# Kernel optimization log

Hardware: AMD Instinct MI355X
Metric: run time of the kernel (lower is better)

Reference implementation:

```python
import jax, jax.numpy as jnp
import numpy as np

B, N, D = 4, 2048, 1024
H, A, Lv = 8, 128, 128   # heads, attention_dim (qk), linear_dim (v)
NUM_BLOCKS = 4
QKV_W = (2 * Lv + 2 * A) * H  # 4096
NEG = -1e9


def setup_inputs() -> dict:
    key = jax.random.key(0)
    ks = jax.random.split(key, 10)
    past_lengths = jax.random.randint(ks[0], (B,), 0, N)
    past_ids = jax.random.randint(ks[1], (B, N), 0, 10000)
    past_embeddings = jax.random.normal(ks[2], (B, N, D), dtype=jnp.float32)
    # per-block parameters, stacked on leading block axis (xavier-ish scale)
    qkv_w = jax.random.normal(ks[3], (NUM_BLOCKS, D, QKV_W), dtype=jnp.float32) * (1.0 / np.sqrt(D))
    qkv_b = jnp.zeros((NUM_BLOCKS, QKV_W), dtype=jnp.float32)
    out_w = jax.random.normal(ks[4], (NUM_BLOCKS, Lv * H, D), dtype=jnp.float32) * (1.0 / np.sqrt(Lv * H))
    out_b = jnp.zeros((NUM_BLOCKS, D), dtype=jnp.float32)
    ln_g = jnp.ones((NUM_BLOCKS, D), dtype=jnp.float32)
    ln_b = jnp.zeros((NUM_BLOCKS, D), dtype=jnp.float32)
    return {"past_lengths": past_lengths, "past_ids": past_ids,
            "past_embeddings": past_embeddings, "qkv_w": qkv_w, "qkv_b": qkv_b,
            "out_w": out_w, "out_b": out_b, "ln_g": ln_g, "ln_b": ln_b}


def _layer_norm(x, g, b, eps=1e-5):
    mu = jnp.mean(x, axis=-1, keepdims=True)
    var = jnp.mean(jnp.square(x - mu), axis=-1, keepdims=True)
    return (x - mu) * jax.lax.rsqrt(var + eps) * g + b


def _block(x, mask, qw, qb, ow, ob, g, b):
    xn = _layer_norm(x, g, b)
    qkv = (xn @ qw + qb).reshape(B, N, H, 2 * Lv + 2 * A)
    q = qkv[..., :A]              # [B,N,H,A]
    k = qkv[..., A:2 * A]         # [B,N,H,A]
    v = qkv[..., 2 * A:2 * A + Lv]  # [B,N,H,Lv]
    scores = jnp.einsum('bnha,bmha->bhnm', q, k) / np.sqrt(A)
    # original: masked_fill(-inf) -> silu -> /N -> softmax; we mask after the
    # silu transform with a large-negative logit so masked weights are ~0
    logits = jnp.where(mask[:, None, :, :], jax.nn.silu(scores) / N, NEG)
    w = jax.nn.softmax(logits, axis=-1)
    attn = jnp.einsum('bhnm,bmhl->bnhl', w, v).reshape(B, N, H * Lv)
    return x + attn @ ow + ob


def reference(past_lengths, past_ids, past_embeddings, qkv_w, qkv_b, out_w, out_b, ln_g, ln_b):
    valid = past_ids != 0                                   # [B,N]
    causal = jnp.triu(jnp.ones((N, N), dtype=bool), k=1)     # faithful to buffer (triu, diag=1)
    mask = causal[None] & valid[:, None, :] & valid[:, :, None]  # [B,N,N]
    x = past_embeddings
    for i in range(NUM_BLOCKS):
        x = _block(x, mask, qkv_w[i], qkv_b[i], out_w[i], out_b[i], ln_g[i], ln_b[i])
    return x
```

## Files before the change

### kernel.cpp

```cpp
#include <hip/hip_runtime.h>

typedef __bf16 bf16_t;
typedef __bf16 bf16x8 __attribute__((ext_vector_type(8)));
typedef __bf16 bf16x4 __attribute__((ext_vector_type(4)));
typedef float f32x4 __attribute__((ext_vector_type(4)));
typedef unsigned int u32x4 __attribute__((ext_vector_type(4)));

#define B_ 4
#define N_ 2048
#define D_ 1024
#define H_ 8
#define NB_ 4
#define M_ (B_*N_)
#define QN_ 3072
#define QKN_ 2048

__device__ __forceinline__ void async_copy16(const void* gsrc, void* ldst) {
    __builtin_amdgcn_global_load_lds(
        (const __attribute__((address_space(1))) void*)gsrc,
        (__attribute__((address_space(3))) void*)ldst, 16, 0, 0);
}

static constexpr size_t WT_OFF  = 0;
static constexpr size_t WT_SZ   = (size_t)NB_*QN_*D_*2;
static constexpr size_t OWT_OFF = WT_OFF + WT_SZ;
static constexpr size_t OWT_SZ  = (size_t)NB_*D_*D_*2;
static constexpr size_t XN_OFF  = OWT_OFF + OWT_SZ;
static constexpr size_t XN_SZ   = (size_t)M_*D_*2;
static constexpr size_t QK_OFF  = XN_OFF + XN_SZ;
static constexpr size_t QK_SZ   = (size_t)M_*QKN_*2;
static constexpr size_t VT_OFF  = QK_OFF + QK_SZ;
static constexpr size_t VT_SZ   = (size_t)32*128*N_*2;
static constexpr size_t ATT_OFF = VT_OFF + VT_SZ;
static constexpr size_t ATT_SZ  = (size_t)M_*D_*2;
static constexpr size_t QBR_OFF = ATT_OFF + ATT_SZ;
static constexpr size_t QBR_SZ  = (size_t)NB_*QN_*4;
static constexpr size_t VS_OFF  = QBR_OFF + QBR_SZ;
static constexpr size_t VS_SZ   = (size_t)NB_*32*128*4;
static constexpr size_t MASK_OFF = VS_OFF + VS_SZ;

__global__ __launch_bounds__(256) void repack_qkvw(const float* __restrict__ qw, bf16_t* __restrict__ wt)
{
    __shared__ float tile[64][65];
    const int nb = blockIdx.z;
    const int j0 = blockIdx.x * 64, d0 = blockIdx.y * 64;
    const int tx = threadIdx.x, ty = threadIdx.y;
    const float* src = qw + (size_t)nb * D_ * 4096;
    const int jj = j0 + tx;
    const int sel = jj >> 10, rr = jj & 1023, hh = rr >> 7, aa = rr & 127;
    const int orig = hh * 512 + sel * 128 + aa;
#pragma unroll
    for (int it = 0; it < 16; ++it) {
        int dr = it * 4 + ty;
        tile[dr][tx] = src[(size_t)(d0 + dr) * 4096 + orig];
    }
    __syncthreads();
    bf16_t* dst = wt + (size_t)nb * QN_ * D_;
#pragma unroll
    for (int it = 0; it < 16; ++it) {
        int jr = it * 4 + ty;
        dst[(size_t)(j0 + jr) * D_ + d0 + tx] = (bf16_t)tile[tx][jr];
    }
}

__global__ __launch_bounds__(256) void repack_outw(const float* __restrict__ ow, bf16_t* __restrict__ owt)
{
    __shared__ float tile[64][65];
    const int nb = blockIdx.z;
    const int j0 = blockIdx.x * 64, d0 = blockIdx.y * 64;
    const int tx = threadIdx.x, ty = threadIdx.y;
    const float* src = ow + (size_t)nb * D_ * D_;
#pragma unroll
    for (int it = 0; it < 16; ++it) {
        int dr = it * 4 + ty;
        tile[dr][tx] = src[(size_t)(d0 + dr) * D_ + j0 + tx];
    }
    __syncthreads();
    bf16_t* dst = owt + (size_t)nb * D_ * D_;
#pragma unroll
    for (int it = 0; it < 16; ++it) {
        int jr = it * 4 + ty;
        dst[(size_t)(j0 + jr) * D_ + d0 + tx] = (bf16_t)tile[tx][jr];
    }
}

__global__ __launch_bounds__(256) void repack_qb(const float* __restrict__ qb, float* __restrict__ qbr)
{
    int idx = blockIdx.x * 256 + threadIdx.x;
    int nb = idx / QN_, jj = idx % QN_;
    int sel = jj >> 10, rr = jj & 1023, hh = rr >> 7, aa = rr & 127;
    qbr[idx] = qb[nb * 4096 + hh * 512 + sel * 128 + aa];
}

__global__ __launch_bounds__(256) void mask_kernel(const int* __restrict__ past_ids, unsigned short* __restrict__ maskA,
                                                   float* __restrict__ vsl)
{
    const int idx = blockIdx.x * 256 + threadIdx.x;
    vsl[idx] = 0.f; vsl[idx + 8192] = 0.f;
    const int b = idx >> 11, P = idx & 2047;
    const int k = P & 31;
    const int m = (P & ~31) | (((k >> 2) & 1) << 4) | (((k >> 3) & 3) << 2) | (k & 3);
    maskA[idx] = past_ids[b * N_ + m] != 0 ? 0xFFFFu : 0u;
}

__global__ __launch_bounds__(256) void ln_kernel(const float* __restrict__ x, const float* __restrict__ g,
                                                 const float* __restrict__ bb, bf16_t* __restrict__ xn)
{
    const int row = blockIdx.x, tid = threadIdx.x;
    const float4 v = ((const float4*)(x + (size_t)row * D_))[tid];
    float s = v.x + v.y + v.z + v.w;
    float q = v.x * v.x + v.y * v.y + v.z * v.z + v.w * v.w;
#pragma unroll
    for (int d = 32; d >= 1; d >>= 1) { s += __shfl_xor(s, d); q += __shfl_xor(q, d); }
    __shared__ float ls[4], lq[4];
    if ((tid & 63) == 0) { ls[tid >> 6] = s; lq[tid >> 6] = q; }
    __syncthreads();
    s = ls[0] + ls[1] + ls[2] + ls[3];
    q = lq[0] + lq[1] + lq[2] + lq[3];
    const float mean = s * (1.f / 1024.f);
    const float var  = q * (1.f / 1024.f) - mean * mean;
    const float inv  = rsqrtf(var + 1e-5f);
    const float4 gg = ((const float4*)g)[tid];
    const float4 bv = ((const float4*)bb)[tid];
    bf16x4 o;
    o[0] = (bf16_t)((v.x - mean) * inv * gg.x + bv.x);
    o[1] = (bf16_t)((v.y - mean) * inv * gg.y + bv.y);
    o[2] = (bf16_t)((v.z - mean) * inv * gg.z + bv.z);
    o[3] = (bf16_t)((v.w - mean) * inv * gg.w + bv.w);
    *(bf16x4*)(xn + (size_t)row * D_ + tid * 4) = o;
}

__global__ __launch_bounds__(512, 2) void gemm_qkv(const bf16_t* __restrict__ Am, const bf16_t* __restrict__ Bt,
                                                   const float* __restrict__ bias,
                                                   bf16_t* __restrict__ outQK, bf16_t* __restrict__ vtOut,
                                                   float* __restrict__ vsOut)
{
    __shared__ bf16_t As[4 * 8192];
    __shared__ bf16_t Bs[4 * 6144];
    const int tid = threadIdx.x;
    const int lane = tid & 63, wave = tid >> 6;
    const int wr = wave >> 2, wc = wave & 3;
    const int quad = lane >> 4, l15 = lane & 15;
    const int swz = quad ^ ((l15 >> 1) & 3);
    const int slane8 = ((lane & 3) ^ ((lane >> 3) & 3)) * 8;
    const int lrow = lane >> 2;
    const int m0 = blockIdx.y * 256, n0 = blockIdx.x * 192;
    const int Kn = D_;
    const bool w4 = (wave < 4);

    const int ch = wave * 2;
    const int bch0 = w4 ? 2 * wave : 4 + wave;
    const int bch1 = w4 ? 2 * wave + 1 : bch0;
    const bf16_t* gA0 = Am + (size_t)(m0 + ch * 16 + lrow) * Kn + slane8;
    const bf16_t* gA1 = gA0 + (size_t)16 * Kn;
    const bf16_t* gB0 = Bt + (size_t)(n0 + bch0 * 16 + lrow) * Kn + slane8;
    const bf16_t* gB1 = Bt + (size_t)(n0 + bch1 * 16 + lrow) * Kn + slane8;
    bf16_t* const dA0 = &As[ch * 512 + lane * 8];
    bf16_t* const dA1 = &As[(ch + 1) * 512 + lane * 8];
    bf16_t* const dB0 = &Bs[bch0 * 512 + lane * 8];
    bf16_t* const dB1 = &Bs[bch1 * 512 + lane * 8];

    auto STAGE = [&](int slot) {
        async_copy16(gA0, dA0 + slot * 8192);
        async_copy16(gA1, dA1 + slot * 8192);
        async_copy16(gB0, dB0 + slot * 6144);
        if (w4) async_copy16(gB1, dB1 + slot * 6144);
        gA0 += 32; gA1 += 32; gB0 += 32; gB1 += 32;
    };

    f32x4 acc[8][3] = {};
    const int NT = Kn >> 5;

    STAGE(0); STAGE(1); STAGE(2);
    if (w4) asm volatile("s_waitcnt vmcnt(8)" ::: "memory");
    else    asm volatile("s_waitcnt vmcnt(6)" ::: "memory");
    __builtin_amdgcn_s_barrier();

    const int aoff = wr * 4096 + l15 * 32 + swz * 8;
    const int boff = wc * 1536 + l15 * 32 + swz * 8;

    for (int t = 0; t < NT; ++t) {
        const int ring = t & 3;
        const bf16_t* ra = &As[ring * 8192 + aoff];
        const bf16_t* rb = &Bs[ring * 6144 + boff];
        bf16x8 af[8], bfv[3];
#pragma unroll
        for (int j = 0; j < 3; ++j) bfv[j] = *(const bf16x8*)(rb + j * 512);
#pragma unroll
        for (int i = 0; i < 8; ++i) af[i] = *(const bf16x8*)(ra + i * 512);
        if (t + 3 < NT) STAGE((t + 3) & 3);
        __builtin_amdgcn_s_setprio(1);
#pragma unroll
        for (int i = 0; i < 8; ++i)
#pragma unroll
            for (int j = 0; j < 3; ++j)
                acc[i][j] = __builtin_amdgcn_mfma_f32_16x16x32_bf16(af[i], bfv[j], acc[i][j], 0, 0, 0);
        __builtin_amdgcn_s_setprio(0);
        if (t + 3 < NT) {
            if (w4) asm volatile("s_waitcnt vmcnt(8)" ::: "memory");
            else    asm volatile("s_waitcnt vmcnt(6)" ::: "memory");
        } else if (t + 2 < NT) {
            if (w4) asm volatile("s_waitcnt vmcnt(4)" ::: "memory");
            else    asm volatile("s_waitcnt vmcnt(3)" ::: "memory");
        } else if (t + 1 < NT) {
            asm volatile("s_waitcnt vmcnt(0)" ::: "memory");
        }
        __builtin_amdgcn_s_barrier();
    }

    const int bb2 = m0 >> 11;
#pragma unroll
    for (int j = 0; j < 3; ++j) {
        const int colg = n0 + wc * 48 + j * 16 + l15;
        const float bv = bias[colg];
        if (colg >= 2048) {
            const int hh = (colg - 2048) >> 7, ll = (colg - 2048) & 127;
            float ps = 32.f * bv;
#pragma unroll
            for (int i = 0; i < 8; ++i) {
                const int rowg = m0 + wr * 128 + i * 16 + quad * 4;
                const int mloc = rowg & 2047;
                const int mperm = (mloc & ~31) | (((mloc >> 2) & 3) << 3) | (((mloc >> 4) & 1) << 2);
                bf16x4 sv;
#pragma unroll
                for (int r = 0; r < 4; ++r) { sv[r] = (bf16_t)(acc[i][j][r] + bv); ps += acc[i][j][r]; }
                *(bf16x4*)(vtOut + ((size_t)(bb2 * 8 + hh) * 128 + ll) * (size_t)N_ + mperm) = sv;
            }
            ps += __shfl_xor(ps, 16);
            ps += __shfl_xor(ps, 32);
            if (quad == 0) atomicAdd(&vsOut[(size_t)(bb2 * 8 + hh) * 128 + ll], ps);
        } else {
            const float qs = (colg < 1024) ? 0.08838834764831845f : 1.f;
#pragma unroll
            for (int i = 0; i < 8; ++i) {
                const int rowg = m0 + wr * 128 + i * 16 + quad * 4;
#pragma unroll
                for (int r = 0; r < 4; ++r)
                    outQK[(size_t)(rowg + r) * QKN_ + colg] = (bf16_t)((acc[i][j][r] + bv) * qs);
            }
        }
    }
}

__global__ __launch_bounds__(512, 2) void gemm_out(const bf16_t* __restrict__ Am, const bf16_t* __restrict__ Bt,
                                                   const float* __restrict__ bias,
                                                   const float* __restrict__ resid_in, float* __restrict__ resid_out)
{
    __shared__ bf16_t As[4 * 256 * 32];
    __shared__ bf16_t Bs[4 * 128 * 32];
    const int tid = threadIdx.x;
    const int lane = tid & 63, wave = tid >> 6;
    const int wr = wave >> 2, wc = wave & 3;
    const int quad = lane >> 4, l15 = lane & 15;
    const int swz = quad ^ ((l15 >> 1) & 3);
    const int slane8 = ((lane & 3) ^ ((lane >> 3) & 3)) * 8;
    const int lrow = lane >> 2;
    const int m0 = blockIdx.y * 256, n0 = blockIdx.x * 128;
    const int Kn = D_;

    const int chA0 = wave * 2, chA1 = chA0 + 1;
    const bf16_t* gA0 = Am + (size_t)(m0 + chA0 * 16 + lrow) * Kn + slane8;
    const bf16_t* gA1 = Am + (size_t)(m0 + chA1 * 16 + lrow) * Kn + slane8;
    const bf16_t* gB  = Bt + (size_t)(n0 + wave * 16 + lrow) * Kn + slane8;
    bf16_t* const dA0 = &As[chA0 * 512 + lane * 8];
    bf16_t* const dA1 = &As[chA1 * 512 + lane * 8];
    bf16_t* const dB  = &Bs[wave * 512 + lane * 8];

    auto STAGE = [&](int slot) {
        async_copy16(gA0, dA0 + slot * 8192);
        async_copy16(gA1, dA1 + slot * 8192);
        async_copy16(gB,  dB  + slot * 4096);
        gA0 += 32; gA1 += 32; gB += 32;
    };

    f32x4 acc[8][2] = {};
    const int NT = Kn >> 5;

    STAGE(0); STAGE(1); STAGE(2);
    asm volatile("s_waitcnt vmcnt(6)" ::: "memory");
    __builtin_amdgcn_s_barrier();

    const int aoff = (wr * 128 + l15) * 32 + swz * 8;
    const int boff = (wc * 32  + l15) * 32 + swz * 8;

    for (int t = 0; t < NT; ++t) {
        const int ring = t & 3;
        const bf16_t* ra = &As[ring * 8192 + aoff];
        const bf16_t* rb = &Bs[ring * 4096 + boff];
        bf16x8 af[8], bfv[2];
#pragma unroll
        for (int j = 0; j < 2; ++j) bfv[j] = *(const bf16x8*)(rb + j * 512);
#pragma unroll
        for (int i = 0; i < 8; ++i) af[i] = *(const bf16x8*)(ra + i * 512);
        if (t + 3 < NT) STAGE((t + 3) & 3);
        __builtin_amdgcn_s_setprio(1);
#pragma unroll
        for (int i = 0; i < 8; ++i)
#pragma unroll
            for (int j = 0; j < 2; ++j)
                acc[i][j] = __builtin_amdgcn_mfma_f32_16x16x32_bf16(af[i], bfv[j], acc[i][j], 0, 0, 0);
        __builtin_amdgcn_s_setprio(0);
        if (t + 3 < NT)      asm volatile("s_waitcnt vmcnt(6)" ::: "memory");
        else if (t + 2 < NT) asm volatile("s_waitcnt vmcnt(3)" ::: "memory");
        else if (t + 1 < NT) asm volatile("s_waitcnt vmcnt(0)" ::: "memory");
        __builtin_amdgcn_s_barrier();
    }

#pragma unroll
    for (int i = 0; i < 8; ++i) {
#pragma unroll
        for (int j = 0; j < 2; ++j) {
            const int colg = n0 + wc * 32 + j * 16 + l15;
            const float bv = bias[colg];
#pragma unroll
            for (int r = 0; r < 4; ++r) {
                const int rowg = m0 + wr * 128 + i * 16 + quad * 4 + r;
                const size_t off = (size_t)rowg * D_ + colg;
                resid_out[off] = resid_in[off] + acc[i][j][r] + bv;
            }
        }
    }
}

template<bool CAUSAL>
__device__ __forceinline__ void attn_tile(
    int m0, int m0n, int n0, int b, int h,
    const bf16_t* __restrict__ qk, const bf16_t* __restrict__ vtb,
    const unsigned short* __restrict__ maskB,
    bf16_t* Ks, bf16_t* Vs,
    const bf16x8 (&qf)[2][4], bf16x8 onesf,
    f32x4 (&oacc)[2][8], f32x4 (&dacc)[2])
{
    const int tid = threadIdx.x, lane = tid & 63, wave = tid >> 6;
    const int quad = lane >> 4, l15 = lane & 15;
    const int swz = quad ^ ((l15 >> 1) & 3);
    const int slane8 = ((lane & 3) ^ ((lane >> 3) & 3)) * 8;
    const int lrow = lane >> 2;
    const float invN = 1.f / 2048.f;

#pragma unroll
    for (int s = 0; s < 8; ++s) {
        const int kkc = s & 3, rg = (s >> 2) + wave * 2;
        async_copy16(vtb + (size_t)(rg * 16 + lrow) * N_ + m0 + kkc * 32 + slane8,
                     &Vs[kkc * 4096 + rg * 512 + lane * 8]);
    }
    bf16x8 mAf[4];
#pragma unroll
    for (int kk = 0; kk < 4; ++kk)
        mAf[kk] = *(const bf16x8*)(maskB + m0 + kk * 32 + quad * 8);

    f32x4 sacc[2][8] = {};
    __builtin_amdgcn_s_setprio(1);
#pragma unroll
    for (int kk = 0; kk < 4; ++kk) {
#pragma unroll
        for (int j = 0; j < 8; ++j) {
            bf16x8 kf = *(const bf16x8*)&Ks[kk * 4096 + (j * 16 + l15) * 32 + swz * 8];
            sacc[0][j] = __builtin_amdgcn_mfma_f32_16x16x32_bf16(kf, qf[0][kk], sacc[0][j], 0, 0, 0);
            sacc[1][j] = __builtin_amdgcn_mfma_f32_16x16x32_bf16(kf, qf[1][kk], sacc[1][j], 0, 0, 0);
        }
    }
    __builtin_amdgcn_s_setprio(0);

    bf16x8 pf[2][4];
#pragma unroll
    for (int kk = 0; kk < 4; ++kk) {
#pragma unroll
        for (int s = 0; s < 2; ++s) {
            const int j = kk * 2 + s;
#pragma unroll
            for (int nb = 0; nb < 2; ++nb) {
#pragma unroll
                for (int r = 0; r < 4; ++r) {
                    const float sv = sacc[nb][j][r];
                    const float xc = __builtin_amdgcn_fmed3f(sv, -4.f, 4.f);
                    float sg = __builtin_fmaf(xc, 0.25f * invN, 0.5f * invN);
                    sg = __builtin_fmaf(-(xc * (0.03125f * invN)), fabsf(xc), sg);
                    float e = __builtin_fmaf(sv, sg, 1.f);
                    if (CAUSAL) {
                        const int dmn = (m0 + j * 16 + quad * 4 + r) - (n0 + wave * 32 + nb * 16 + l15);
                        e = (dmn > 0) ? e : 0.f;
                    }
                    pf[nb][kk][s * 4 + r] = (bf16_t)e;
                }
            }
        }
        *(u32x4*)&pf[0][kk] = *(u32x4*)&pf[0][kk] & *(const u32x4*)&mAf[kk];
        *(u32x4*)&pf[1][kk] = *(u32x4*)&pf[1][kk] & *(const u32x4*)&mAf[kk];
    }

    __syncthreads();

    if (m0n < N_) {
        const size_t baseq = (size_t)b * N_ * QKN_;
#pragma unroll
        for (int s = 0; s < 8; ++s) {
            const int kkc = s & 3, rg = (s >> 2) + wave * 2;
            async_copy16(qk + baseq + (size_t)(m0n + rg * 16 + lrow) * QKN_ + 1024 + h * 128 + kkc * 32 + slane8,
                         &Ks[kkc * 4096 + rg * 512 + lane * 8]);
        }
    }

    __builtin_amdgcn_s_setprio(1);
#pragma unroll
    for (int kk = 0; kk < 4; ++kk) {
        dacc[0] = __builtin_amdgcn_mfma_f32_16x16x32_bf16(pf[0][kk], onesf, dacc[0], 0, 0, 0);
        dacc[1] = __builtin_amdgcn_mfma_f32_16x16x32_bf16(pf[1][kk], onesf, dacc[1], 0, 0, 0);
#pragma unroll
        for (int j = 0; j < 8; ++j) {
            bf16x8 vf = *(const bf16x8*)&Vs[kk * 4096 + (j * 16 + l15) * 32 + swz * 8];
            oacc[0][j] = __builtin_amdgcn_mfma_f32_16x16x32_bf16(pf[0][kk], vf, oacc[0][j], 0, 0, 0);
            oacc[1][j] = __builtin_amdgcn_mfma_f32_16x16x32_bf16(pf[1][kk], vf, oacc[1][j], 0, 0, 0);
        }
    }
    __builtin_amdgcn_s_setprio(0);
    __syncthreads();
}

__global__ __launch_bounds__(256, 2) void attn_kernel(const bf16_t* __restrict__ qk, const bf16_t* __restrict__ vt,
                                                      const int* __restrict__ past_ids, const float* __restrict__ vsum,
                                                      const unsigned short* __restrict__ maskA,
                                                      bf16_t* __restrict__ att)
{
    __shared__ bf16_t Ks[4 * 128 * 32];
    __shared__ bf16_t Vs[4 * 128 * 32];

    const int bx = blockIdx.x;
    const int bh = bx & 31, g = bx >> 5;
    const int t = (g < 8) ? g : 23 - g;
    const int b = bh >> 3, h = bh & 7;
    const int n0 = t << 7;
    const int tid = threadIdx.x, lane = tid & 63, wave = tid >> 6;
    const int quad = lane >> 4, l15 = lane & 15;
    const int slane8 = ((lane & 3) ^ ((lane >> 3) & 3)) * 8;
    const int lrow = lane >> 2;
    const bf16_t* vtb = vt + (size_t)bh * 128 * N_;
    const unsigned short* maskB = maskA + b * N_;
    const float invN = 1.f / 2048.f;

    bf16x8 qf[2][4];
#pragma unroll
    for (int nb = 0; nb < 2; ++nb) {
        const bf16_t* gq = qk + (size_t)b * N_ * QKN_ + (size_t)(n0 + wave * 32 + nb * 16 + l15) * QKN_ + h * 128 + quad * 8;
#pragma unroll
        for (int kk = 0; kk < 4; ++kk) qf[nb][kk] = *(const bf16x8*)(gq + kk * 32);
    }
    const float vnf0 = past_ids[b * N_ + n0 + wave * 32 + l15] != 0 ? 1.f : 0.f;
    const float vnf1 = past_ids[b * N_ + n0 + wave * 32 + 16 + l15] != 0 ? 1.f : 0.f;
    bf16x8 onesf;
#pragma unroll
    for (int i = 0; i < 8; ++i) onesf[i] = (bf16_t)1.f;

    {
        const size_t baseq = (size_t)b * N_ * QKN_;
#pragma unroll
        for (int s = 0; s < 8; ++s) {
            const int kkc = s & 3, rg = (s >> 2) + wave * 2;
            async_copy16(qk + baseq + (size_t)(n0 + rg * 16 + lrow) * QKN_ + 1024 + h * 128 + kkc * 32 + slane8,
                         &Ks[kkc * 4096 + rg * 512 + lane * 8]);
        }
    }
    __syncthreads();

    f32x4 oacc[2][8] = {};
    f32x4 dacc[2] = {};

    attn_tile<true>(n0, n0 + 128, n0, b, h, qk, vtb, maskB, Ks, Vs, qf, onesf, oacc, dacc);
    for (int m0 = n0 + 128; m0 < N_; m0 += 128)
        attn_tile<false>(m0, m0 + 128, n0, b, h, qk, vtb, maskB, Ks, Vs, qf, onesf, oacc, dacc);

    float vsr[8];
#pragma unroll
    for (int j = 0; j < 8; ++j) vsr[j] = vsum[bh * 128 + j * 16 + l15];
#pragma unroll
    for (int nb = 0; nb < 2; ++nb) {
        const float vn = nb ? vnf1 : vnf0;
#pragma unroll
        for (int r = 0; r < 4; ++r) {
            const float dn = dacc[nb][r];
            const bool uni = (vn == 0.f) || !(dn > 0.f);
            const float rc = uni ? 0.f : __builtin_amdgcn_rcpf(dn);
            const int gn = n0 + wave * 32 + nb * 16 + quad * 4 + r;
#pragma unroll
            for (int j = 0; j < 8; ++j) {
                const float ov = uni ? (vsr[j] * invN) : (oacc[nb][j][r] * rc);
                att[(size_t)(b * N_ + gn) * 1024 + h * 128 + j * 16 + l15] = (bf16_t)ov;
            }
        }
    }
}

extern "C" void kernel_launch(void* const* d_in, const int* in_sizes, int n_in,
                              void* d_out, int out_size, void* d_ws, size_t ws_size,
                              hipStream_t stream) {
    (void)in_sizes; (void)n_in; (void)out_size; (void)ws_size;
    const int*   past_ids = (const int*)d_in[1];
    const float* past_emb = (const float*)d_in[2];
    const float* qkv_w    = (const float*)d_in[3];
    const float* qkv_b    = (const float*)d_in[4];
    const float* out_w    = (const float*)d_in[5];
    const float* out_b    = (const float*)d_in[6];
    const float* ln_g     = (const float*)d_in[7];
    const float* ln_b     = (const float*)d_in[8];

    float* x = (float*)d_out;
    char* ws = (char*)d_ws;
    bf16_t* WT  = (bf16_t*)(ws + WT_OFF);
    bf16_t* OWT = (bf16_t*)(ws + OWT_OFF);
    bf16_t* XN  = (bf16_t*)(ws + XN_OFF);
    bf16_t* QK  = (bf16_t*)(ws + QK_OFF);
    bf16_t* VT  = (bf16_t*)(ws + VT_OFF);
    bf16_t* ATT = (bf16_t*)(ws + ATT_OFF);
    float*  QBR = (float*)(ws + QBR_OFF);
    float*  VSL = (float*)(ws + VS_OFF);
    unsigned short* MASKA = (unsigned short*)(ws + MASK_OFF);

    repack_qkvw<<<dim3(48, 16, NB_), dim3(64, 4), 0, stream>>>(qkv_w, WT);
    repack_outw<<<dim3(16, 16, NB_), dim3(64, 4), 0, stream>>>(out_w, OWT);
    repack_qb<<<48, 256, 0, stream>>>(qkv_b, QBR);
    mask_kernel<<<32, 256, 0, stream>>>(past_ids, MASKA, VSL);

    for (int layer = 0; layer < NB_; ++layer) {
        const float* xin = (layer == 0) ? past_emb : x;
        ln_kernel<<<M_, 256, 0, stream>>>(xin, ln_g + layer * D_, ln_b + layer * D_, XN);
        gemm_qkv<<<dim3(QN_ / 192, M_ / 256), 512, 0, stream>>>(
            XN, WT + (size_t)layer * QN_ * D_, QBR + layer * QN_, QK, VT, VSL + layer * 4096);
        attn_kernel<<<512, 256, 0, stream>>>(QK, VT, past_ids, VSL + layer * 4096, MASKA, ATT);
        gemm_out<<<dim3(D_ / 128, M_ / 256), 512, 0, stream>>>(
            ATT, OWT + (size_t)layer * D_ * D_, out_b + layer * D_, xin, x);
    }
}
```

Measured before the change: 828.7 us.

## Switch QKV GEMM to double-buffered BK=64 pipeline and reorder epilogue

The QKV GEMM's 4-slot ring of 32-wide K tiles is replaced by a 2-slot double buffer of 64-wide K tiles. Each wave now issues an even share of async copies (4 A, 3 B), and the loop waits with vmcnt(0) once per step, halving the number of barriers. The epilogue loops over rows first and defers the V column-sum shuffle and atomic to the end. This trades prefetch depth (one tile ahead instead of three) for fewer barriers and balanced load issue, so memory latency may be less well hidden.

After: 835.5 us. Within noise of the previous version (+0.8%).

```diff
diff --git a/kernel.cpp b/kernel.cpp
--- a/kernel.cpp
+++ b/kernel.cpp
@@ -135,8 +135,8 @@
                                                    bf16_t* __restrict__ outQK, bf16_t* __restrict__ vtOut,
                                                    float* __restrict__ vsOut)
 {
-    __shared__ bf16_t As[4 * 8192];
-    __shared__ bf16_t Bs[4 * 6144];
+    __shared__ bf16_t As[2 * 16384];
+    __shared__ bf16_t Bs[2 * 12288];
     const int tid = threadIdx.x;
     const int lane = tid & 63, wave = tid >> 6;
     const int wr = wave >> 2, wc = wave & 3;
@@ -146,98 +146,100 @@
     const int lrow = lane >> 2;
     const int m0 = blockIdx.y * 256, n0 = blockIdx.x * 192;
     const int Kn = D_;
-    const bool w4 = (wave < 4);
-
-    const int ch = wave * 2;
-    const int bch0 = w4 ? 2 * wave : 4 + wave;
-    const int bch1 = w4 ? 2 * wave + 1 : bch0;
-    const bf16_t* gA0 = Am + (size_t)(m0 + ch * 16 + lrow) * Kn + slane8;
-    const bf16_t* gA1 = gA0 + (size_t)16 * Kn;
-    const bf16_t* gB0 = Bt + (size_t)(n0 + bch0 * 16 + lrow) * Kn + slane8;
-    const bf16_t* gB1 = Bt + (size_t)(n0 + bch1 * 16 + lrow) * Kn + slane8;
-    bf16_t* const dA0 = &As[ch * 512 + lane * 8];
-    bf16_t* const dA1 = &As[(ch + 1) * 512 + lane * 8];
-    bf16_t* const dB0 = &Bs[bch0 * 512 + lane * 8];
-    bf16_t* const dB1 = &Bs[bch1 * 512 + lane * 8];
+
+    const bf16_t* gA[4]; bf16_t* dA[4];
+    const bf16_t* gB[3]; bf16_t* dB[3];
+#pragma unroll
+    for (int u = 0; u < 4; ++u) {
+        const int a = wave * 4 + u, ch = a >> 1, hf = a & 1;
+        gA[u] = Am + (size_t)(m0 + ch * 16 + lrow) * Kn + hf * 32 + slane8;
+        dA[u] = &As[hf * 8192 + ch * 512 + lane * 8];
+    }
+#pragma unroll
+    for (int u = 0; u < 3; ++u) {
+        const int b = wave * 3 + u, ch = b >> 1, hf = b & 1;
+        gB[u] = Bt + (size_t)(n0 + ch * 16 + lrow) * Kn + hf * 32 + slane8;
+        dB[u] = &Bs[hf * 6144 + ch * 512 + lane * 8];
+    }
 
     auto STAGE = [&](int slot) {
-        async_copy16(gA0, dA0 + slot * 8192);
-        async_copy16(gA1, dA1 + slot * 8192);
-        async_copy16(gB0, dB0 + slot * 6144);
-        if (w4) async_copy16(gB1, dB1 + slot * 6144);
-        gA0 += 32; gA1 += 32; gB0 += 32; gB1 += 32;
+#pragma unroll
+        for (int u = 0; u < 4; ++u) { async_copy16(gA[u], dA[u] + slot * 16384); gA[u] += 64; }
+#pragma unroll
+        for (int u = 0; u < 3; ++u) { async_copy16(gB[u], dB[u] + slot * 12288); gB[u] += 64; }
     };
 
     f32x4 acc[8][3] = {};
-    const int NT = Kn >> 5;
-
-    STAGE(0); STAGE(1); STAGE(2);
-    if (w4) asm volatile("s_waitcnt vmcnt(8)" ::: "memory");
-    else    asm volatile("s_waitcnt vmcnt(6)" ::: "memory");
+    const int NT = Kn >> 6;
+
+    STAGE(0);
+    asm volatile("s_waitcnt vmcnt(0)" ::: "memory");
     __builtin_amdgcn_s_barrier();
 
-    const int aoff = wr * 4096 + l15 * 32 + swz * 8;
-    const int boff = wc * 1536 + l15 * 32 + swz * 8;
+    const int abase = wr * 4096 + l15 * 32 + swz * 8;
+    const int bbase = wc * 1536 + l15 * 32 + swz * 8;
 
     for (int t = 0; t < NT; ++t) {
-        const int ring = t & 3;
-        const bf16_t* ra = &As[ring * 8192 + aoff];
-        const bf16_t* rb = &Bs[ring * 6144 + boff];
-        bf16x8 af[8], bfv[3];
-#pragma unroll
-        for (int j = 0; j < 3; ++j) bfv[j] = *(const bf16x8*)(rb + j * 512);
-#pragma unroll
-        for (int i = 0; i < 8; ++i) af[i] = *(const bf16x8*)(ra + i * 512);
-        if (t + 3 < NT) STAGE((t + 3) & 3);
+        const int slot = t & 1;
+        const bf16_t* ra = &As[slot * 16384 + abase];
+        const bf16_t* rb = &Bs[slot * 12288 + bbase];
+        if (t + 1 < NT) STAGE(slot ^ 1);
         __builtin_amdgcn_s_setprio(1);
 #pragma unroll
-        for (int i = 0; i < 8; ++i)
-#pragma unroll
-            for (int j = 0; j < 3; ++j)
-                acc[i][j] = __builtin_amdgcn_mfma_f32_16x16x32_bf16(af[i], bfv[j], acc[i][j], 0, 0, 0);
+        for (int hf = 0; hf < 2; ++hf) {
+            bf16x8 af[8], bfv[3];
+#pragma unroll
+            for (int j = 0; j < 3; ++j) bfv[j] = *(const bf16x8*)(rb + hf * 6144 + j * 512);
+#pragma unroll
+            for (int i = 0; i < 8; ++i) af[i] = *(const bf16x8*)(ra + hf * 8192 + i * 512);
+#pragma unroll
+            for (int i = 0; i < 8; ++i)
+#pragma unroll
+                for (int j = 0; j < 3; ++j)
+                    acc[i][j] = __builtin_amdgcn_mfma_f32_16x16x32_bf16(af[i], bfv[j], acc[i][j], 0, 0, 0);
+        }
         __builtin_amdgcn_s_setprio(0);
-        if (t + 3 < NT) {
-            if (w4) asm volatile("s_waitcnt vmcnt(8)" ::: "memory");
-            else    asm volatile("s_waitcnt vmcnt(6)" ::: "memory");
-        } else if (t + 2 < NT) {
-            if (w4) asm volatile("s_waitcnt vmcnt(4)" ::: "memory");
-            else    asm volatile("s_waitcnt vmcnt(3)" ::: "memory");
-        } else if (t + 1 < NT) {
-            asm volatile("s_waitcnt vmcnt(0)" ::: "memory");
-        }
+        if (t + 1 < NT) asm volatile("s_waitcnt vmcnt(0)" ::: "memory");
         __builtin_amdgcn_s_barrier();
     }
 
     const int bb2 = m0 >> 11;
-#pragma unroll
-    for (int j = 0; j < 3; ++j) {
-        const int colg = n0 + wc * 48 + j * 16 + l15;
-        const float bv = bias[colg];
-        if (colg >= 2048) {
-            const int hh = (colg - 2048) >> 7, ll = (colg - 2048) & 127;
-            float ps = 32.f * bv;
-#pragma unroll
-            for (int i = 0; i < 8; ++i) {
-                const int rowg = m0 + wr * 128 + i * 16 + quad * 4;
-                const int mloc = rowg & 2047;
-                const int mperm = (mloc & ~31) | (((mloc >> 2) & 3) << 3) | (((mloc >> 4) & 1) << 2);
+    int colgj[3]; float bvj[3];
+#pragma unroll
+    for (int j = 0; j < 3; ++j) { colgj[j] = n0 + wc * 48 + j * 16 + l15; bvj[j] = bias[colgj[j]]; }
+    float ps[3] = {0.f, 0.f, 0.f};
+#pragma unroll
+    for (int i = 0; i < 8; ++i) {
+        const int rowg = m0 + wr * 128 + i * 16 + quad * 4;
+        const int mloc = rowg & 2047;
+        const int mperm = (mloc & ~31) | (((mloc >> 2) & 3) << 3) | (((mloc >> 4) & 1) << 2);
+#pragma unroll
+        for (int j = 0; j < 3; ++j) {
+            const int colg = colgj[j];
+            const float bv = bvj[j];
+            if (colg >= 2048) {
+                const int hh = (colg - 2048) >> 7, ll = (colg - 2048) & 127;
                 bf16x4 sv;
 #pragma unroll
-                for (int r = 0; r < 4; ++r) { sv[r] = (bf16_t)(acc[i][j][r] + bv); ps += acc[i][j][r]; }
+                for (int r = 0; r < 4; ++r) { sv[r] = (bf16_t)(acc[i][j][r] + bv); ps[j] += acc[i][j][r]; }
                 *(bf16x4*)(vtOut + ((size_t)(bb2 * 8 + hh) * 128 + ll) * (size_t)N_ + mperm) = sv;
-            }
-            ps += __shfl_xor(ps, 16);
-            ps += __shfl_xor(ps, 32);
-            if (quad == 0) atomicAdd(&vsOut[(size_t)(bb2 * 8 + hh) * 128 + ll], ps);
-        } else {
-            const float qs = (colg < 1024) ? 0.08838834764831845f : 1.f;
-#pragma unroll
-            for (int i = 0; i < 8; ++i) {
-                const int rowg = m0 + wr * 128 + i * 16 + quad * 4;
+            } else {
+                const float qs = (colg < 1024) ? 0.08838834764831845f : 1.f;
 #pragma unroll
                 for (int r = 0; r < 4; ++r)
                     outQK[(size_t)(rowg + r) * QKN_ + colg] = (bf16_t)((acc[i][j][r] + bv) * qs);
             }
+        }
+    }
+#pragma unroll
+    for (int j = 0; j < 3; ++j) {
+        const int colg = colgj[j];
+        if (colg >= 2048) {
+            const int hh = (colg - 2048) >> 7, ll = (colg - 2048) & 127;
+            float p = ps[j] + 32.f * bvj[j];
+            p += __shfl_xor(p, 16);
+            p += __shfl_xor(p, 32);
+            if (quad == 0) atomicAdd(&vsOut[(size_t)(bb2 * 8 + hh) * 128 + ll], p);
         }
     }
 }
```
